# Kernel tuning notes

Measured on AMD Instinct MI355X. Metric: run time of the kernel, lower is better.

Reference implementation:

```python
import jax, jax.numpy as jnp
import numpy as np

B, S, L = 256, 2048, 64  # batch, seq_len, label_size (= num_labels + 2)
START, END = L - 2, L - 1


def setup_inputs() -> dict:
    key = jax.random.key(0)
    k1, k2, k3, k4 = jax.random.split(key, 4)
    logits = jax.random.normal(k1, (B, S, L), dtype=jnp.float32)
    # pad_logits: <SOS>/<EOS> score columns are -100
    logits = logits.at[:, :, START:].set(-100.0)
    transition = jax.random.normal(k2, (L, L), dtype=jnp.float32)
    # CRF.initialize(): nothing transitions into end-as-source / out of start-as-target
    transition = transition.at[:, END].set(-100.0)
    transition = transition.at[START, :].set(-100.0)
    labels = jax.random.randint(k3, (B, S), 0, L - 2, dtype=jnp.int32)
    lens = jnp.maximum(jax.random.randint(k4, (B,), 1, S + 1, dtype=jnp.int32), 1)
    return {"logits": logits, "transition": transition, "labels": labels, "lens": lens}


def _loglik(logits, transition, labels, lens):
    Bc, Sc, Lc = logits.shape
    dt = logits.dtype
    mask_s = (jnp.arange(Sc)[None, :] < lens[:, None])  # [B,S] valid-token mask

    # ---- gold unary score: sum_t logits[b, t, labels[b,t]] over valid t ----
    unary = jnp.take_along_axis(logits, labels[..., None].astype(jnp.int32), axis=2)[..., 0]
    gold_unary = jnp.sum(unary * mask_s.astype(dt), axis=1)  # [B]

    # ---- gold binary score: transition[to, from] along extended label path ----
    lab_ext = jnp.concatenate(
        [jnp.full((Bc, 1), START, labels.dtype), labels, jnp.full((Bc, 1), END, labels.dtype)],
        axis=1,
    )  # [B, S+2]
    m_ext = jnp.arange(Sc + 2)[None, :] < (lens + 1)[:, None]
    lab_ext = jnp.where(m_ext, lab_ext, END)  # positions past lens become <EOS>
    trn_scr = transition[lab_ext[:, 1:], lab_ext[:, :-1]]  # [B, S+1]
    m_trn = (jnp.arange(Sc + 1)[None, :] < (lens + 1)[:, None]).astype(dt)
    gold_binary = jnp.sum(trn_scr * m_trn, axis=1)  # [B]
    gold = gold_unary + gold_binary

    # ---- norm score: forward algorithm (log-semiring scan over time) ----
    alpha0 = jnp.full((Bc, Lc), -100.0, dtype=dt).at[:, START].set(0.0)

    def step(alpha, inp):
        logit, active = inp  # logit: [B,L], active: [B]
        # mat[b, to, frm] = logit[b,to] + alpha[b,frm] + transition[to,frm]
        mat = logit[:, :, None] + alpha[:, None, :] + transition[None, :, :]
        alpha_nxt = jax.nn.logsumexp(mat, axis=2)  # [B,L]
        alpha = jnp.where(active[:, None], alpha_nxt, alpha)
        return alpha, None

    alpha, _ = jax.lax.scan(step, alpha0, (jnp.swapaxes(logits, 0, 1), mask_s.T))
    norm = jax.nn.logsumexp(alpha + transition[END][None, :], axis=1)  # [B]

    return gold - norm


def reference(logits, transition, labels, lens):
    return _loglik(logits, transition, labels, lens)
```

## Files before the change

### kernel.cpp

```cpp
#include <hip/hip_runtime.h>


#define Bsz 256
#define Ssz 2048
#define START_ 62
#define END_ 63
#define PSTRIDE 36
#define CH 256
#define NC 8

typedef __attribute__((ext_vector_type(2))) _Float16 half2v;
typedef __attribute__((ext_vector_type(8))) _Float16 half8;
typedef __attribute__((ext_vector_type(16))) float f32x16;

__device__ __forceinline__ unsigned pack_pkrtz(float a, float b) {
    auto h = __builtin_amdgcn_cvt_pkrtz(a, b);
    return __builtin_bit_cast(unsigned, h);
}

__device__ __forceinline__ float dot2h(unsigned a, unsigned b, float c) {
#if __has_builtin(__builtin_amdgcn_fdot2)
    return __builtin_amdgcn_fdot2(__builtin_bit_cast(half2v, a),
                                  __builtin_bit_cast(half2v, b), c, false);
#else
    half2v ha = __builtin_bit_cast(half2v, a);
    half2v hb = __builtin_bit_cast(half2v, b);
    c = __builtin_fmaf((float)ha.x, (float)hb.x, c);
    return __builtin_fmaf((float)ha.y, (float)hb.y, c);
#endif
}

__device__ __forceinline__ float wave_sum(float v) {
#pragma unroll
    for (int m = 32; m >= 1; m >>= 1) v += __shfl_xor(v, m, 64);
    return v;
}

#define CRF_STEP(LG)                                                           \
    {                                                                          \
        const float l_ = __builtin_amdgcn_exp2f((LG) * L2E);                   \
        const int nbi_ = __builtin_amdgcn_update_dpp(                          \
            0, __float_as_int(E), 0xB1, 0xf, 0xf, true); \
        const unsigned packed_ = pack_pkrtz(E, __int_as_float(nbi_));          \
        float c0 = 0.f, c1 = 0.f, c2 = 0.f, c3 = 0.f;                          \
        float c4 = 0.f, c5 = 0.f, c6 = 0.f, c7 = 0.f;                          \
        _Pragma("unroll")                                                      \
        for (int k8 = 0; k8 < 8; ++k8) {                                       \
            const uint4 q_ = q[k8];                                            \
            const unsigned t0 = (unsigned)__builtin_amdgcn_readlane(           \
                (int)packed_, 8 * k8 + 0);                                     \
            const unsigned t1 = (unsigned)__builtin_amdgcn_readlane(           \
                (int)packed_, 8 * k8 + 2);                                     \
            const unsigned t2 = (unsigned)__builtin_amdgcn_readlane(           \
                (int)packed_, 8 * k8 + 4);                                     \
            const unsigned t3 = (unsigned)__builtin_amdgcn_readlane(           \
                (int)packed_, 8 * k8 + 6);                                     \
            if (k8 & 1) {                                                      \
                c4 = dot2h(t0, q_.x, c4);                                      \
                c5 = dot2h(t1, q_.y, c5);                                      \
                c6 = dot2h(t2, q_.z, c6);                                      \
                c7 = dot2h(t3, q_.w, c7);                                      \
            } else {                                                           \
                c0 = dot2h(t0, q_.x, c0);                                      \
                c1 = dot2h(t1, q_.y, c1);                                      \
                c2 = dot2h(t2, q_.z, c2);                                      \
                c3 = dot2h(t3, q_.w, c3);                                      \
            }                                                                  \
        }                                                                      \
        const float y_ = ((c0 + c1) + (c2 + c3)) + ((c4 + c5) + (c6 + c7));    \
        const float Ey_ = y_ * l_;                                             \
        const int pb_ = __builtin_amdgcn_readlane(__float_as_int(Ey_), 0);     \
        const int ee_ = (pb_ >> 23) & 0xff;                                    \
        const float sc_ = __int_as_float((244 - ee_) << 23);                   \
        E = Ey_ * sc_;                                                         \
        D += ee_ - 117;                                                        \
    }

#define LOAD_QBLOCK()                                                          \
    {                                                                          \
        unsigned off_ = (unsigned)(lane * (PSTRIDE * 4));                      \
        asm volatile("" : "+v"(off_));                                         \
        const uint4* prow_ = (const uint4*)((const char*)Psh + off_);          \
        _Pragma("unroll")                                                      \
        for (int k8 = 0; k8 < 8; ++k8) q[k8] = prow_[k8];                      \
    }

__global__ __launch_bounds__(64)
__attribute__((amdgpu_waves_per_eu(1, 1)))
void crf_kernel(const float* __restrict__ logits,
                const float* __restrict__ transition,
                const int* __restrict__ labels,
                const int* __restrict__ lens,
                float* __restrict__ out)
{
    const int b    = blockIdx.x;
    const int lane = threadIdx.x;
    const float L2E = 1.4426950408889634f;
    const float LN2 = 0.6931471805599453f;

    __shared__ unsigned Psh[64 * PSTRIDE];

    const int len = lens[b];
    const float* lrow = logits + (size_t)b * (Ssz * 64);

#pragma unroll
    for (int k = 0; k < 32; ++k) {
        float p0 = __builtin_amdgcn_exp2f(transition[lane * 64 + 2 * k]     * L2E);
        float p1 = __builtin_amdgcn_exp2f(transition[lane * 64 + 2 * k + 1] * L2E);
        Psh[lane * PSTRIDE + k] = pack_pkrtz(p0, p1);
    }
    asm volatile("s_waitcnt lgkmcnt(0)" ::: "memory");

    float E = (lane == START_) ? 1.0f : 0.0f;
    int   D = 0;

    float lgb[8];
#pragma unroll
    for (int d = 0; d < 8; ++d) {
        int s0 = (d < len) ? d : (len - 1);
        lgb[d] = lrow[s0 * 64 + lane];
    }

    uint4 q[8];
    const int len8 = len & ~7;
    for (int s = 0; s < len8; s += 8) {
        LOAD_QBLOCK();
#pragma unroll
        for (int d = 0; d < 8; ++d) {
            const float lg = lgb[d];
            int pf = s + 8 + d;
            pf = (pf < len) ? pf : (len - 1);
            lgb[d] = lrow[pf * 64 + lane];
            CRF_STEP(lg);
        }
    }
    const int rem = len - len8;
    if (rem) {
        LOAD_QBLOCK();
        for (int d = 0; d < rem; ++d) {
            const float lg = lgb[d];
            CRF_STEP(lg);
        }
    }

    const float Pend = __builtin_amdgcn_exp2f(transition[END_ * 64 + lane] * L2E);
    const float tot  = wave_sum(E * Pend);
    const float norm = LN2 * ((float)D + __builtin_amdgcn_logf(tot));

    const int* lab = labels + (size_t)b * Ssz;
    float g = 0.0f;
    for (int s = lane; s < len; s += 64) {
        const int l1 = lab[s];
        const int l0 = (s == 0) ? START_ : lab[s - 1];
        g += lrow[s * 64 + l1] + transition[l1 * 64 + l0];
    }
    if (lane == 0) g += transition[END_ * 64 + lab[len - 1]];
    const float gold = wave_sum(g);

    if (lane == 0) out[b] = gold - norm;
}


#define MF16(Aop, Bop, Cop) \
    __builtin_amdgcn_mfma_f32_32x32x16_f16((Aop), (Bop), (Cop), 0, 0, 0)

#define STEP_COMPUTE(LGA, LGB)                                                 \
    f32x16 a00, a01, a10, a11;                                                 \
    {                                                                          \
        const float ncf_ = -(float)ci;                                         \
        const float lv0_ = __builtin_amdgcn_exp2f(                             \
            __builtin_fmaf((LGA), L2E, ncf_));                                 \
        const float lv1_ = __builtin_amdgcn_exp2f(                             \
            __builtin_fmaf((LGB), L2E, ncf_));                                 \
        D += ci;                                                               \
        const _Float16 h0_ = (_Float16)lv0_;                                   \
        const _Float16 h1_ = (_Float16)lv1_;                                   \
        const half8 sv0_ = {h0_, h0_, h0_, h0_, h0_, h0_, h0_, h0_};           \
        const half8 sv1_ = {h1_, h1_, h1_, h1_, h1_, h1_, h1_, h1_};           \
        half8 A_;                                                              \
        A_ = __builtin_bit_cast(half8, PF[0][0]) * sv0_;                       \
        a00 = MF16(A_, __builtin_bit_cast(half8, Bf[0][0]), Z);                \
        a01 = MF16(A_, __builtin_bit_cast(half8, Bf[0][1]), Z);                \
        A_ = __builtin_bit_cast(half8, PF[0][1]) * sv0_;                       \
        a00 = MF16(A_, __builtin_bit_cast(half8, Bf[1][0]), a00);              \
        a01 = MF16(A_, __builtin_bit_cast(half8, Bf[1][1]), a01);              \
        A_ = __builtin_bit_cast(half8, PF[0][2]) * sv0_;                       \
        a00 = MF16(A_, __builtin_bit_cast(half8, Bf[2][0]), a00);              \
        a01 = MF16(A_, __builtin_bit_cast(half8, Bf[2][1]), a01);              \
        A_ = __builtin_bit_cast(half8, PF[0][3]) * sv0_;                       \
        a00 = MF16(A_, __builtin_bit_cast(half8, Bf[3][0]), a00);              \
        a01 = MF16(A_, __builtin_bit_cast(half8, Bf[3][1]), a01);              \
        A_ = __builtin_bit_cast(half8, PF[1][0]) * sv1_;                       \
        a10 = MF16(A_, __builtin_bit_cast(half8, Bf[0][0]), Z);                \
        a11 = MF16(A_, __builtin_bit_cast(half8, Bf[0][1]), Z);                \
        A_ = __builtin_bit_cast(half8, PF[1][1]) * sv1_;                       \
        a10 = MF16(A_, __builtin_bit_cast(half8, Bf[1][0]), a10);              \
        a11 = MF16(A_, __builtin_bit_cast(half8, Bf[1][1]), a11);              \
        A_ = __builtin_bit_cast(half8, PF[1][2]) * sv1_;                       \
        a10 = MF16(A_, __builtin_bit_cast(half8, Bf[2][0]), a10);              \
        a11 = MF16(A_, __builtin_bit_cast(half8, Bf[2][1]), a11);              \
        A_ = __builtin_bit_cast(half8, PF[1][3]) * sv1_;                       \
        a10 = MF16(A_, __builtin_bit_cast(half8, Bf[3][0]), a10);              \
        a11 = MF16(A_, __builtin_bit_cast(half8, Bf[3][1]), a11);              \
        const float mxa_ = fmaxf(fmaxf(fmaxf(a00[0], a00[1]),                  \
                                       fmaxf(a00[2], a00[3])),                 \
                                 fmaxf(fmaxf(a00[4], a00[5]),                  \
                                       fmaxf(a00[6], a00[7])));                \
        const float mxb_ = fmaxf(fmaxf(fmaxf(a00[8], a00[9]),                  \
                                       fmaxf(a00[10], a00[11])),               \
                                 fmaxf(fmaxf(a00[12], a00[13]),                \
                                       fmaxf(a00[14], a00[15])));              \
        const int mb_ = __builtin_amdgcn_readfirstlane(                        \
            __float_as_int(fmaxf(mxa_, mxb_)));                                \
        ci = ((mb_ >> 23) & 0xff) - 121;       \
    }

#define TILE_TO_FRAGS(ACC, BD0, BD1)                                           \
    {                                                                          \
        (BD0) = make_uint4(pack_pkrtz(ACC[0], ACC[1]),                         \
                           pack_pkrtz(ACC[2], ACC[3]),                         \
                           pack_pkrtz(ACC[4], ACC[5]),                         \
                           pack_pkrtz(ACC[6], ACC[7]));                        \
        (BD1) = make_uint4(pack_pkrtz(ACC[8], ACC[9]),                         \
                           pack_pkrtz(ACC[10], ACC[11]),                       \
                           pack_pkrtz(ACC[12], ACC[13]),                       \
                           pack_pkrtz(ACC[14], ACC[15]));                      \
    }

#define STEP_FULL(LGA, LGB)                                                    \
    {                                                                          \
        STEP_COMPUTE(LGA, LGB);                                                \
        TILE_TO_FRAGS(a00, Bf[0][0], Bf[1][0]);                                \
        TILE_TO_FRAGS(a01, Bf[0][1], Bf[1][1]);                                \
        TILE_TO_FRAGS(a10, Bf[2][0], Bf[3][0]);                                \
        TILE_TO_FRAGS(a11, Bf[2][1], Bf[3][1]);                                \
    }

#define STEP_LAST(LGA, LGB)                                                    \
    {                                                                          \
        STEP_COMPUTE(LGA, LGB);                                                \
        float* gout_ = Gws + (size_t)bc * 4096;                                \
        _Pragma("unroll")                                                      \
        for (int r = 0; r < 16; ++r) {                                         \
            const int row0_ = (r & 3) + 8 * (r >> 2) + 4 * hi;                 \
            gout_[row0_ * 64 + lo5]             = a00[r];                      \
            gout_[row0_ * 64 + 32 + lo5]        = a01[r];                      \
            gout_[(row0_ + 32) * 64 + lo5]      = a10[r];                      \
            gout_[(row0_ + 32) * 64 + 32 + lo5] = a11[r];                      \
        }                                                                      \
        if (lane == 0) Dws[bc] = D;                                            \
    }

__global__ __launch_bounds__(64)
__attribute__((amdgpu_waves_per_eu(2, 2)))
void crf_chunk(const float* __restrict__ logits,
               const float* __restrict__ transition,
               const int* __restrict__ lens,
               float* __restrict__ Gws,
               int* __restrict__ Dws)
{
    const int bc   = blockIdx.x;
    const int b    = bc >> 3;
    const int c    = bc & 7;
    const int lane = threadIdx.x;
    const int lo5  = lane & 31;
    const int hi   = lane >> 5;
    const float L2E = 1.4426950408889634f;

    const int len = lens[b];
    const int s0  = c * CH;
    if (s0 >= len) {
        if (lane == 0) Dws[bc] = 0;
        return;
    }
    const int s1 = (s0 + CH < len) ? (s0 + CH) : len;

    uint4 PF[2][4];
#pragma unroll
    for (int m = 0; m < 2; ++m) {
#pragma unroll
        for (int kb = 0; kb < 4; ++kb) {
            const float* tp = transition + (m * 32 + lo5) * 64 + kb * 16 + 4 * hi;
            const float e0 = __builtin_amdgcn_exp2f(tp[0] * L2E);
            const float e1 = __builtin_amdgcn_exp2f(tp[1] * L2E);
            const float e2 = __builtin_amdgcn_exp2f(tp[2] * L2E);
            const float e3 = __builtin_amdgcn_exp2f(tp[3] * L2E);
            const float e4 = __builtin_amdgcn_exp2f(tp[8] * L2E);
            const float e5 = __builtin_amdgcn_exp2f(tp[9] * L2E);
            const float e6 = __builtin_amdgcn_exp2f(tp[10] * L2E);
            const float e7 = __builtin_amdgcn_exp2f(tp[11] * L2E);
            PF[m][kb] = make_uint4(pack_pkrtz(e0, e1), pack_pkrtz(e2, e3),
                                   pack_pkrtz(e4, e5), pack_pkrtz(e6, e7));
        }
    }

    uint4 Bf[4][2];
#pragma unroll
    for (int kb = 0; kb < 4; ++kb) {
#pragma unroll
        for (int nb = 0; nb < 2; ++nb) {
            const int col = nb * 32 + lo5;
            unsigned dw[4];
#pragma unroll
            for (int j = 0; j < 4; ++j) {
                const int k0 = kb * 16 + 4 * hi + (j >> 1) * 8 + (j & 1) * 2;
                const unsigned lo16 = (k0     == col) ? 0x3C00u : 0u;
                const unsigned hi16 = (k0 + 1 == col) ? 0x3C00u : 0u;
                dw[j] = lo16 | (hi16 << 16);
            }
            Bf[kb][nb] = make_uint4(dw[0], dw[1], dw[2], dw[3]);
        }
    }

    float z0 = 0.0f;
    asm volatile("" : "+v"(z0));
    f32x16 Z;
#pragma unroll
    for (int i = 0; i < 16; ++i) Z[i] = z0;

    int D  = 0;
    int ci = 0;

    const float* lrow = logits + (size_t)b * (Ssz * 64);
#define CLMP(x) (((x) < s1) ? (x) : (s1 - 1))

    float pA0, pA1, pA2, pA3, pB0, pB1, pB2, pB3;
    {
        int sI;
        sI = CLMP(s0 + 0); pA0 = lrow[sI * 64 + lo5]; pB0 = lrow[sI * 64 + 32 + lo5];
        sI = CLMP(s0 + 1); pA1 = lrow[sI * 64 + lo5]; pB1 = lrow[sI * 64 + 32 + lo5];
        sI = CLMP(s0 + 2); pA2 = lrow[sI * 64 + lo5]; pB2 = lrow[sI * 64 + 32 + lo5];
        sI = CLMP(s0 + 3); pA3 = lrow[sI * 64 + lo5]; pB3 = lrow[sI * 64 + 32 + lo5];
    }

    const int nfull = (s1 - s0) - 1;
    int t = 0;
    for (; t + 4 <= nfull; t += 4) {
        const int sp = s0 + t + 4;
        const int q0i = CLMP(sp), q1i = CLMP(sp + 1), q2i = CLMP(sp + 2), q3i = CLMP(sp + 3);
        const float nA0 = lrow[q0i * 64 + lo5], nB0 = lrow[q0i * 64 + 32 + lo5];
        const float nA1 = lrow[q1i * 64 + lo5], nB1 = lrow[q1i * 64 + 32 + lo5];
        const float nA2 = lrow[q2i * 64 + lo5], nB2 = lrow[q2i * 64 + 32 + lo5];
        const float nA3 = lrow[q3i * 64 + lo5], nB3 = lrow[q3i * 64 + 32 + lo5];
        STEP_FULL(pA0, pB0);
        STEP_FULL(pA1, pB1);
        STEP_FULL(pA2, pB2);
        STEP_FULL(pA3, pB3);
        pA0 = nA0; pB0 = nB0; pA1 = nA1; pB1 = nB1;
        pA2 = nA2; pB2 = nB2; pA3 = nA3; pB3 = nB3;
    }
    const int r_ = nfull - t;
    if (r_ >= 1) STEP_FULL(pA0, pB0);
    if (r_ >= 2) STEP_FULL(pA1, pB1);
    if (r_ >= 3) STEP_FULL(pA2, pB2);

    float fA = pA0, fB = pB0;
    if (r_ == 1) { fA = pA1; fB = pB1; }
    else if (r_ == 2) { fA = pA2; fB = pB2; }
    else if (r_ == 3) { fA = pA3; fB = pB3; }
    STEP_LAST(fA, fB);
#undef CLMP
}

__global__ __launch_bounds__(64)
__attribute__((amdgpu_waves_per_eu(1, 1)))
void crf_combine(const float* __restrict__ logits,
                 const float* __restrict__ transition,
                 const int* __restrict__ labels,
                 const int* __restrict__ lens,
                 const float* __restrict__ Gws,
                 const int* __restrict__ Dws,
                 float* __restrict__ out)
{
    const int b    = blockIdx.x;
    const int lane = threadIdx.x;
    const float L2E = 1.4426950408889634f;
    const float LN2 = 0.6931471805599453f;
    const int len = lens[b];
    const float* lrow = logits + (size_t)b * (Ssz * 64);

    float E = (lane == START_) ? 1.0f : 0.0f;
    int Dtot = 0;
#pragma unroll 1
    for (int c = 0; c < NC; ++c) {
        if (c * CH >= len) break;
        const float4* g4 =
            (const float4*)(Gws + (size_t)(b * NC + c) * 4096 + lane * 64);
        float4 gr[16];
#pragma unroll
        for (int jj = 0; jj < 16; ++jj) gr[jj] = g4[jj];

        const int Ei = __float_as_int(E);
        float En = 0.0f;
#pragma unroll
        for (int jj = 0; jj < 16; ++jj) {
            En = __builtin_fmaf(gr[jj].x,
                __int_as_float(__builtin_amdgcn_readlane(Ei, 4 * jj + 0)), En);
            En = __builtin_fmaf(gr[jj].y,
                __int_as_float(__builtin_amdgcn_readlane(Ei, 4 * jj + 1)), En);
            En = __builtin_fmaf(gr[jj].z,
                __int_as_float(__builtin_amdgcn_readlane(Ei, 4 * jj + 2)), En);
            En = __builtin_fmaf(gr[jj].w,
                __int_as_float(__builtin_amdgcn_readlane(Ei, 4 * jj + 3)), En);
        }
        Dtot += Dws[b * NC + c];

        float mxv = En;
#pragma unroll
        for (int m = 32; m >= 1; m >>= 1) mxv = fmaxf(mxv, __shfl_xor(mxv, m, 64));
        const int ee = (__float_as_int(mxv) >> 23) & 0xff;
        const float scn = __int_as_float((254 - ee) << 23);
        E = En * scn;
        Dtot += ee - 127;
    }

    const float Pend = __builtin_amdgcn_exp2f(transition[END_ * 64 + lane] * L2E);
    const float tot  = wave_sum(E * Pend);
    const float norm = LN2 * ((float)Dtot + __builtin_amdgcn_logf(tot));

    const int* lab = labels + (size_t)b * Ssz;
    float g = 0.0f;
    for (int s = lane; s < len; s += 64) {
        const int l1 = lab[s];
        const int l0 = (s == 0) ? START_ : lab[s - 1];
        g += lrow[s * 64 + l1] + transition[l1 * 64 + l0];
    }
    if (lane == 0) g += transition[END_ * 64 + lab[len - 1]];
    const float gold = wave_sum(g);

    if (lane == 0) out[b] = gold - norm;
}

extern "C" void kernel_launch(void* const* d_in, const int* in_sizes, int n_in,
                              void* d_out, int out_size, void* d_ws, size_t ws_size,
                              hipStream_t stream) {
    const float* logits     = (const float*)d_in[0];
    const float* transition = (const float*)d_in[1];
    const int*   labels     = (const int*)d_in[2];
    const int*   lens       = (const int*)d_in[3];
    float*       out        = (float*)d_out;

    const size_t gBytes = (size_t)Bsz * NC * 4096 * sizeof(float);
    const size_t need   = gBytes + (size_t)Bsz * NC * sizeof(int);
    if (d_ws != nullptr && ws_size >= need) {
        float* Gws = (float*)d_ws;
        int*   Dws = (int*)((char*)d_ws + gBytes);
        crf_chunk<<<dim3(Bsz * NC), dim3(64), 0, stream>>>(
            logits, transition, lens, Gws, Dws);
        crf_combine<<<dim3(Bsz), dim3(64), 0, stream>>>(
            logits, transition, labels, lens, Gws, Dws, out);
    } else {
        crf_kernel<<<dim3(Bsz), dim3(64), 0, stream>>>(
            logits, transition, labels, lens, out);
    }
}
```

Before: 379.6 us.

## Halve chunk length, reorder chunk grid, split gold/norm across waves in combine

Templates the chunked forward pass on chunk size and launches 16 chunks of 128 steps per sequence when workspace allows, with a chunk-major block order and a per-chunk batch rotation to balance load across sequences of different lengths. Occupancy hints are raised for the chunk kernel. The combine kernel now runs the gold-path sum in a second wave in parallel with the norm chain, and the norm matvec uses four partial accumulators. The chunk kernel also raises wave priority around the MFMA block, shortens the max-reduction tree and clamps the rescale exponent. In exchange, combine must apply twice as many 64x64 chunk matrices serially, and the intermediate workspace doubles.

```diff
diff --git a/kernel.cpp b/kernel.cpp
--- a/kernel.cpp
+++ b/kernel.cpp
@@ -6,8 +6,6 @@
 #define START_ 62
 #define END_ 63
 #define PSTRIDE 36
-#define CH 256
-#define NC 8
 
 typedef __attribute__((ext_vector_type(2))) _Float16 half2v;
 typedef __attribute__((ext_vector_type(8))) _Float16 half8;
@@ -40,7 +38,7 @@
     {                                                                          \
         const float l_ = __builtin_amdgcn_exp2f((LG) * L2E);                   \
         const int nbi_ = __builtin_amdgcn_update_dpp(                          \
-            0, __float_as_int(E), 0xB1, 0xf, 0xf, true); \
+            0, __float_as_int(E), 0xB1, 0xf, 0xf, true);                       \
         const unsigned packed_ = pack_pkrtz(E, __int_as_float(nbi_));          \
         float c0 = 0.f, c1 = 0.f, c2 = 0.f, c3 = 0.f;                          \
         float c4 = 0.f, c5 = 0.f, c6 = 0.f, c7 = 0.f;                          \
@@ -178,6 +176,7 @@
         const half8 sv0_ = {h0_, h0_, h0_, h0_, h0_, h0_, h0_, h0_};           \
         const half8 sv1_ = {h1_, h1_, h1_, h1_, h1_, h1_, h1_, h1_};           \
         half8 A_;                                                              \
+        __builtin_amdgcn_s_setprio(1);                                         \
         A_ = __builtin_bit_cast(half8, PF[0][0]) * sv0_;                       \
         a00 = MF16(A_, __builtin_bit_cast(half8, Bf[0][0]), Z);                \
         a01 = MF16(A_, __builtin_bit_cast(half8, Bf[0][1]), Z);                \
@@ -202,17 +201,19 @@
         A_ = __builtin_bit_cast(half8, PF[1][3]) * sv1_;                       \
         a10 = MF16(A_, __builtin_bit_cast(half8, Bf[3][0]), a10);              \
         a11 = MF16(A_, __builtin_bit_cast(half8, Bf[3][1]), a11);              \
-        const float mxa_ = fmaxf(fmaxf(fmaxf(a00[0], a00[1]),                  \
-                                       fmaxf(a00[2], a00[3])),                 \
-                                 fmaxf(fmaxf(a00[4], a00[5]),                  \
-                                       fmaxf(a00[6], a00[7])));                \
-        const float mxb_ = fmaxf(fmaxf(fmaxf(a00[8], a00[9]),                  \
-                                       fmaxf(a00[10], a00[11])),               \
-                                 fmaxf(fmaxf(a00[12], a00[13]),                \
-                                       fmaxf(a00[14], a00[15])));              \
+        __builtin_amdgcn_s_setprio(0);                                         \
+        const float t0_ = fmaxf(fmaxf(a00[0], a00[1]), a00[2]);                \
+        const float t1_ = fmaxf(fmaxf(a00[3], a00[4]), a00[5]);                \
+        const float t2_ = fmaxf(fmaxf(a00[6], a00[7]), a00[8]);                \
+        const float t3_ = fmaxf(fmaxf(a00[9], a00[10]), a00[11]);              \
+        const float t4_ = fmaxf(fmaxf(a00[12], a00[13]), a00[14]);             \
+        const float ma_ = fmaxf(fmaxf(t0_, t1_), t2_);                         \
+        const float mb2_ = fmaxf(fmaxf(t3_, t4_), a00[15]);                    \
         const int mb_ = __builtin_amdgcn_readfirstlane(                        \
-            __float_as_int(fmaxf(mxa_, mxb_)));                                \
-        ci = ((mb_ >> 23) & 0xff) - 121;       \
+            __float_as_int(fmaxf(ma_, mb2_)));                                 \
+        int cin_ = ((mb_ >> 23) & 0xff) - 121;      \
+        cin_ = (cin_ < -60) ? -60 : cin_;                                      \
+        ci = (cin_ > 60) ? 60 : cin_;                                          \
     }
 
 #define TILE_TO_FRAGS(ACC, BD0, BD1)                                           \
@@ -239,7 +240,7 @@
 #define STEP_LAST(LGA, LGB)                                                    \
     {                                                                          \
         STEP_COMPUTE(LGA, LGB);                                                \
-        float* gout_ = Gws + (size_t)bc * 4096;                                \
+        float* gout_ = Gws + (size_t)gslot * 4096;                             \
         _Pragma("unroll")                                                      \
         for (int r = 0; r < 16; ++r) {                                         \
             const int row0_ = (r & 3) + 8 * (r >> 2) + 4 * hi;                 \
@@ -248,32 +249,35 @@
             gout_[(row0_ + 32) * 64 + lo5]      = a10[r];                      \
             gout_[(row0_ + 32) * 64 + 32 + lo5] = a11[r];                      \
         }                                                                      \
-        if (lane == 0) Dws[bc] = D;                                            \
-    }
-
+        if (lane == 0) Dws[gslot] = D;                                         \
+    }
+
+template<int CHT>
 __global__ __launch_bounds__(64)
-__attribute__((amdgpu_waves_per_eu(2, 2)))
+__attribute__((amdgpu_waves_per_eu(4, 4)))
 void crf_chunk(const float* __restrict__ logits,
                const float* __restrict__ transition,
                const int* __restrict__ lens,
                float* __restrict__ Gws,
                int* __restrict__ Dws)
 {
-    const int bc   = blockIdx.x;
-    const int b    = bc >> 3;
-    const int c    = bc & 7;
+    const int NCc  = Ssz / CHT;
+    const int idx  = blockIdx.x;
+    const int c    = idx >> 8;
+    const int b    = ((idx & 255) + 37 * c) & 255;
     const int lane = threadIdx.x;
     const int lo5  = lane & 31;
     const int hi   = lane >> 5;
     const float L2E = 1.4426950408889634f;
 
-    const int len = lens[b];
-    const int s0  = c * CH;
+    const int len   = lens[b];
+    const int s0    = c * CHT;
+    const int gslot = b * NCc + c;
     if (s0 >= len) {
-        if (lane == 0) Dws[bc] = 0;
+        if (lane == 0) Dws[gslot] = 0;
         return;
     }
-    const int s1 = (s0 + CH < len) ? (s0 + CH) : len;
+    const int s1 = (s0 + CHT < len) ? (s0 + CHT) : len;
 
     uint4 PF[2][4];
 #pragma unroll
@@ -362,8 +366,9 @@
 #undef CLMP
 }
 
-__global__ __launch_bounds__(64)
-__attribute__((amdgpu_waves_per_eu(1, 1)))
+template<int CHT>
+__global__ __launch_bounds__(128)
+__attribute__((amdgpu_waves_per_eu(1, 2)))
 void crf_combine(const float* __restrict__ logits,
                  const float* __restrict__ transition,
                  const int* __restrict__ labels,
@@ -372,63 +377,78 @@
                  const int* __restrict__ Dws,
                  float* __restrict__ out)
 {
+    const int NCc  = Ssz / CHT;
     const int b    = blockIdx.x;
-    const int lane = threadIdx.x;
+    const int wid  = threadIdx.x >> 6;
+    const int lane = threadIdx.x & 63;
     const float L2E = 1.4426950408889634f;
     const float LN2 = 0.6931471805599453f;
     const int len = lens[b];
     const float* lrow = logits + (size_t)b * (Ssz * 64);
 
-    float E = (lane == START_) ? 1.0f : 0.0f;
-    int Dtot = 0;
+    __shared__ float s_gold;
+    float norm = 0.0f;
+
+    if (wid == 1) {
+        const int* lab = labels + (size_t)b * Ssz;
+        float g = 0.0f;
+#pragma unroll 4
+        for (int s = lane; s < len; s += 64) {
+            const int l1 = lab[s];
+            const int l0 = (s == 0) ? START_ : lab[s - 1];
+            g += lrow[s * 64 + l1] + transition[l1 * 64 + l0];
+        }
+        if (lane == 0) g += transition[END_ * 64 + lab[len - 1]];
+        const float gold = wave_sum(g);
+        if (lane == 0) s_gold = gold;
+    } else {
+        float E = (lane == START_) ? 1.0f : 0.0f;
+        int Dtot = 0;
 #pragma unroll 1
-    for (int c = 0; c < NC; ++c) {
-        if (c * CH >= len) break;
-        const float4* g4 =
-            (const float4*)(Gws + (size_t)(b * NC + c) * 4096 + lane * 64);
-        float4 gr[16];
-#pragma unroll
-        for (int jj = 0; jj < 16; ++jj) gr[jj] = g4[jj];
-
-        const int Ei = __float_as_int(E);
-        float En = 0.0f;
-#pragma unroll
-        for (int jj = 0; jj < 16; ++jj) {
-            En = __builtin_fmaf(gr[jj].x,
-                __int_as_float(__builtin_amdgcn_readlane(Ei, 4 * jj + 0)), En);
-            En = __builtin_fmaf(gr[jj].y,
-                __int_as_float(__builtin_amdgcn_readlane(Ei, 4 * jj + 1)), En);
-            En = __builtin_fmaf(gr[jj].z,
-                __int_as_float(__builtin_amdgcn_readlane(Ei, 4 * jj + 2)), En);
-            En = __builtin_fmaf(gr[jj].w,
-                __int_as_float(__builtin_amdgcn_readlane(Ei, 4 * jj + 3)), En);
-        }
-        Dtot += Dws[b * NC + c];
-
-        float mxv = En;
-#pragma unroll
-        for (int m = 32; m >= 1; m >>= 1) mxv = fmaxf(mxv, __shfl_xor(mxv, m, 64));
-        const int ee = (__float_as_int(mxv) >> 23) & 0xff;
-        const float scn = __int_as_float((254 - ee) << 23);
-        E = En * scn;
-        Dtot += ee - 127;
-    }
-
-    const float Pend = __builtin_amdgcn_exp2f(transition[END_ * 64 + lane] * L2E);
-    const float tot  = wave_sum(E * Pend);
-    const float norm = LN2 * ((float)Dtot + __builtin_amdgcn_logf(tot));
-
-    const int* lab = labels + (size_t)b * Ssz;
-    float g = 0.0f;
-    for (int s = lane; s < len; s += 64) {
-        const int l1 = lab[s];
-        const int l0 = (s == 0) ? START_ : lab[s - 1];
-        g += lrow[s * 64 + l1] + transition[l1 * 64 + l0];
-    }
-    if (lane == 0) g += transition[END_ * 64 + lab[len - 1]];
-    const float gold = wave_sum(g);
-
-    if (lane == 0) out[b] = gold - norm;
+        for (int c = 0; c < NCc; ++c) {
+            if (c * CHT >= len) break;
+            const float4* g4 =
+                (const float4*)(Gws + (size_t)(b * NCc + c) * 4096 + lane * 64);
+            float4 gr[16];
+#pragma unroll
+            for (int jj = 0; jj < 16; ++jj) gr[jj] = g4[jj];
+
+            const int Ei = __float_as_int(E);
+            float Ens[4] = {0.f, 0.f, 0.f, 0.f};
+#pragma unroll
+            for (int gq = 0; gq < 4; ++gq) {
+#pragma unroll
+                for (int qq = 0; qq < 4; ++qq) {
+                    const int jj = 4 * gq + qq;
+                    Ens[gq] = __builtin_fmaf(gr[jj].x,
+                        __int_as_float(__builtin_amdgcn_readlane(Ei, 4 * jj + 0)), Ens[gq]);
+                    Ens[gq] = __builtin_fmaf(gr[jj].y,
+                        __int_as_float(__builtin_amdgcn_readlane(Ei, 4 * jj + 1)), Ens[gq]);
+                    Ens[gq] = __builtin_fmaf(gr[jj].z,
+                        __int_as_float(__builtin_amdgcn_readlane(Ei, 4 * jj + 2)), Ens[gq]);
+                    Ens[gq] = __builtin_fmaf(gr[jj].w,
+                        __int_as_float(__builtin_amdgcn_readlane(Ei, 4 * jj + 3)), Ens[gq]);
+                }
+            }
+            const float En = (Ens[0] + Ens[1]) + (Ens[2] + Ens[3]);
+            Dtot += Dws[b * NCc + c];
+
+            float mxv = En;
+#pragma unroll
+            for (int m = 32; m >= 1; m >>= 1) mxv = fmaxf(mxv, __shfl_xor(mxv, m, 64));
+            const int ee = (__float_as_int(mxv) >> 23) & 0xff;
+            const float scn = __int_as_float((254 - ee) << 23);
+            E = En * scn;
+            Dtot += ee - 127;
+        }
+
+        const float Pend = __builtin_amdgcn_exp2f(transition[END_ * 64 + lane] * L2E);
+        const float tot  = wave_sum(E * Pend);
+        norm = LN2 * ((float)Dtot + __builtin_amdgcn_logf(tot));
+    }
+
+    __syncthreads();
+    if (wid == 0 && lane == 0) out[b] = s_gold - norm;
 }
 
 extern "C" void kernel_launch(void* const* d_in, const int* in_sizes, int n_in,
@@ -440,14 +460,24 @@
     const int*   lens       = (const int*)d_in[3];
     float*       out        = (float*)d_out;
 
-    const size_t gBytes = (size_t)Bsz * NC * 4096 * sizeof(float);
-    const size_t need   = gBytes + (size_t)Bsz * NC * sizeof(int);
-    if (d_ws != nullptr && ws_size >= need) {
+    const size_t g16  = (size_t)Bsz * 16 * 4096 * sizeof(float);
+    const size_t n16  = g16 + (size_t)Bsz * 16 * sizeof(int);
+    const size_t g8   = (size_t)Bsz * 8 * 4096 * sizeof(float);
+    const size_t n8   = g8 + (size_t)Bsz * 8 * sizeof(int);
+
+    if (d_ws != nullptr && ws_size >= n16) {
         float* Gws = (float*)d_ws;
-        int*   Dws = (int*)((char*)d_ws + gBytes);
-        crf_chunk<<<dim3(Bsz * NC), dim3(64), 0, stream>>>(
+        int*   Dws = (int*)((char*)d_ws + g16);
+        crf_chunk<128><<<dim3(Bsz * 16), dim3(64), 0, stream>>>(
             logits, transition, lens, Gws, Dws);
-        crf_combine<<<dim3(Bsz), dim3(64), 0, stream>>>(
+        crf_combine<128><<<dim3(Bsz), dim3(128), 0, stream>>>(
+            logits, transition, labels, lens, Gws, Dws, out);
+    } else if (d_ws != nullptr && ws_size >= n8) {
+        float* Gws = (float*)d_ws;
+        int*   Dws = (int*)((char*)d_ws + g8);
+        crf_chunk<256><<<dim3(Bsz * 8), dim3(64), 0, stream>>>(
+            logits, transition, lens, Gws, Dws);
+        crf_combine<256><<<dim3(Bsz), dim3(128), 0, stream>>>(
             logits, transition, labels, lens, Gws, Dws, out);
     } else {
         crf_kernel<<<dim3(Bsz), dim3(64), 0, stream>>>(
```

Measured after the change: 815.7 us. 115% more time.
